# Kernel optimization log

Measured on AMD Instinct MI355X. Metric: run time of the kernel, lower is better.

## Reference

```python
import jax, jax.numpy as jnp
import numpy as np

BS, L, D, K, G, E = 512, 128, 512, 30, 8, 2048
H = E // 2  # MLP hidden = embed_dim // 2


def setup_inputs():
    key = jax.random.key(0)
    ks = jax.random.split(key, 8)
    features = jax.random.normal(ks[0], (BS, L, D), jnp.float32)
    atten = jax.random.uniform(ks[1], (BS, L, L), jnp.float32)
    rng = np.random.default_rng(0)
    lens = rng.integers(34, L - 1, size=BS)          # caption lengths (>= 34 so lengths-2 > K)
    toks = rng.integers(1, 1000, size=(BS, L))
    pos = np.arange(L)[None, :]
    text = np.where(pos < lens[:, None], toks, 0)    # zero padding
    text[np.arange(BS), lens - 1] = 49407            # eos = max token id -> argmax finds it
    text = jnp.asarray(text, jnp.int32)
    pid = jnp.asarray(np.repeat(np.arange(BS // G), G), jnp.int32)  # 64 groups of size G=8
    dlp_w = jax.random.normal(ks[2], (G, D), jnp.float32)           # weights['weight_8']
    dlp_b = jnp.zeros((G,), jnp.float32)                            # biases['bias_8']
    dlp_lw = jax.random.normal(ks[3], (K * G, E), jnp.float32) * 0.05  # linears['linear_8']
    dlp_lb = jnp.zeros((E,), jnp.float32)
    mlp_w1 = jax.random.normal(ks[4], (D, H), jnp.float32) * 0.04
    mlp_b1 = jnp.zeros((H,), jnp.float32)
    bn_g = jnp.ones((H,), jnp.float32)
    bn_b = jnp.zeros((H,), jnp.float32)
    mlp_w2 = jax.random.normal(ks[5], (H, E), jnp.float32) * 0.03
    mlp_b2 = jnp.zeros((E,), jnp.float32)
    return dict(features=features, atten=atten, text=text, pid=pid,
                dlp_w=dlp_w, dlp_b=dlp_b, dlp_lw=dlp_lw, dlp_lb=dlp_lb,
                mlp_w1=mlp_w1, mlp_b1=mlp_b1, bn_g=bn_g, bn_b=bn_b,
                mlp_w2=mlp_w2, mlp_b2=mlp_b2)


def _l2norm(x, eps=1e-8):
    return x / (jnp.sqrt(jnp.sum(x * x, axis=-1, keepdims=True)) + eps)


def _groups_from_pid(pid_np):
    # replicates the pid_dist==0 grouping + dedup-by-member-set, preserving first-seen order
    groups, order = {}, []
    for i, p in enumerate(pid_np.tolist()):
        if p not in groups:
            groups[p] = []
            order.append(p)
        groups[p].append(i)
    return [groups[p] for p in order]


def reference(features, atten, text, pid, dlp_w, dlp_b, dlp_lw, dlp_lb,
              mlp_w1, mlp_b1, bn_g, bn_b, mlp_w2, mlp_b2):
    bs = features.shape[0]
    b = jnp.arange(bs)
    mask = (text != 0).astype(features.dtype)                  # [bs, L]
    lengths = mask.sum(1) - 2.0                                # [bs]
    eos = jnp.argmax(text, axis=-1)                            # [bs]
    att = atten.at[b, :, eos].set(-1.0).at[:, :, 0].set(-1.0)
    row = att[b, eos, :] * mask                                # [bs, L]
    idx = jax.lax.top_k(row, K)[1]                             # [bs, K] topk token indices
    feats = jnp.take_along_axis(features, idx[:, :, None], axis=1)  # [bs, K, D]

    # pid-based dynamic grouping (host-side; pid is an index input, static)
    glists = _groups_from_pid(np.asarray(pid))
    assert {len(g) for g in glists} == {G}, 'expert params provided for group size G only'
    gi = np.asarray(glists)                                    # [ng, G]
    xg = feats[gi].reshape(gi.shape[0], G * K, D)              # concat group members: [ng, G*K, D]
    # F.linear(x, W[G,D], b).T  ->  [ng, G, G*K]
    h = jnp.einsum('ntd,gd->ngt', xg, dlp_w) + dlp_b[None, :, None]
    yg = h @ dlp_lw + dlp_lb                                   # linear_G: [ng, G, E]
    # scatter-combine each member's row back to its batch position
    new_base = jnp.zeros((bs, E), feats.dtype).at[gi.reshape(-1)].set(yg.reshape(-1, E))
    new_base = _l2norm(new_base)

    # MLP (Linear -> BatchNorm1d(train stats) -> ReLU -> Linear) on l2-normed gathered feats
    x = _l2norm(feats).reshape(bs * K, D) @ mlp_w1 + mlp_b1
    mu, var = x.mean(0), x.var(0)
    x = jax.nn.relu((x - mu) / jnp.sqrt(var + 1e-5) * bn_g + bn_b)
    x = (x @ mlp_w2 + mlp_b2).reshape(bs, K, E)

    # maxk_pool1d_var with pool k=1: per-channel max over first min(length, K) rows
    lens = jnp.minimum(lengths, K).astype(jnp.int32)
    valid = jnp.arange(K)[None, :] < lens[:, None]             # [bs, K]
    pooled = jnp.max(jnp.where(valid[:, :, None], x, -jnp.inf), axis=1)  # [bs, E]
    return (pooled + new_base).astype(jnp.float32)
```

## Files before the change

kernel.cpp:

```cpp
#include <hip/hip_runtime.h>
#include <hip/hip_bf16.h>

#define BS 512
#define LL 128
#define DD 512
#define KK 30
#define GG 8
#define EE 2048
#define HH 1024
#define NROWS (BS*KK)
#define NG (BS/GG)

typedef __attribute__((ext_vector_type(8))) short bf16x8;
typedef __attribute__((ext_vector_type(4))) float f32x4;
typedef __attribute__((address_space(1))) const unsigned int gu32;
typedef __attribute__((address_space(3))) unsigned int lu32;

__device__ __forceinline__ unsigned short f2bf(float f){
  unsigned int x = __float_as_uint(f);
  x = (x + 0x7FFFu + ((x >> 16) & 1u)) >> 16;
  return (unsigned short)x;
}
__device__ __forceinline__ float bf2f(unsigned short u){
  return __uint_as_float(((unsigned int)u) << 16);
}
__device__ __forceinline__ unsigned fkey(float f){
  unsigned b = __float_as_uint(f);
  return (b & 0x80000000u) ? ~b : (b | 0x80000000u);
}
__device__ __forceinline__ float fdec(unsigned k){
  unsigned b = (k & 0x80000000u) ? (k & 0x7FFFFFFFu) : ~k;
  return __uint_as_float(b);
}

__global__ __launch_bounds__(64) void k_prep(const float* __restrict__ atten,
                                             const int* __restrict__ text,
                                             int* __restrict__ idx,
                                             int* __restrict__ lensk){
  const int b = blockIdx.x;
  const int lane = threadIdx.x;
  const int t0 = text[b*LL + lane];
  const int t1 = text[b*LL + 64 + lane];

  int v, vi;
  if(t1 > t0){ v = t1; vi = lane + 64; } else { v = t0; vi = lane; }
#pragma unroll
  for(int off = 32; off; off >>= 1){
    const int ov = __shfl_xor(v, off), oi = __shfl_xor(vi, off);
    if(ov > v || (ov == v && oi < vi)){ v = ov; vi = oi; }
  }
  const int eos = vi;

  const unsigned long long mb0 = __ballot(t0 != 0), mb1 = __ballot(t1 != 0);
  if(lane == 0) lensk[b] = min(__popcll(mb0) + __popcll(mb1) - 2, KK);

  const float a0 = atten[(size_t)b*LL*LL + (size_t)eos*LL + lane];
  const float a1 = atten[(size_t)b*LL*LL + (size_t)eos*LL + 64 + lane];
  float r0 = (t0 == 0) ? 0.f : ((lane == 0 || lane == eos) ? -1.f : a0);
  float r1 = (t1 == 0) ? 0.f : ((lane + 64 == eos) ? -1.f : a1);

  for(int k = 0; k < KK; k++){
    float mv; int mi;
    if(r1 > r0){ mv = r1; mi = lane + 64; } else { mv = r0; mi = lane; }
#pragma unroll
    for(int off = 32; off; off >>= 1){
      const float ov = __shfl_xor(mv, off); const int oi = __shfl_xor(mi, off);
      if(ov > mv || (ov == mv && oi < mi)){ mv = ov; mi = oi; }
    }
    if(lane == 0) idx[b*KK + k] = mi;
    if(mi == lane)      r0 = -3.f;
    if(mi == lane + 64) r1 = -3.f;
  }
}

__global__ __launch_bounds__(128) void k_gather(const float* __restrict__ features,
                                                const float* __restrict__ dlp_w,
                                                const float* __restrict__ dlp_b,
                                                const int* __restrict__ idx,
                                                unsigned short* __restrict__ nfeats,
                                                float* __restrict__ hval){
  const int r = blockIdx.x;
  const int b = r / KK;
  const int t = threadIdx.x;
  const int l = idx[r];

  const float4 v = ((const float4*)features)[((size_t)b*LL + l)*(DD/4) + t];
  float ss = v.x*v.x + v.y*v.y + v.z*v.z + v.w*v.w;
  float hg[GG];
#pragma unroll
  for(int g = 0; g < GG; g++){
    const float4 w = ((const float4*)dlp_w)[g*(DD/4) + t];
    hg[g] = v.x*w.x + v.y*w.y + v.z*w.z + v.w*w.w;
  }
#pragma unroll
  for(int off = 32; off > 0; off >>= 1){
    ss += __shfl_down(ss, off);
#pragma unroll
    for(int g = 0; g < GG; g++) hg[g] += __shfl_down(hg[g], off);
  }
  __shared__ float red[2][9];
  __shared__ float s_rn;
  const int wave = t >> 6, lane = t & 63;
  if(lane == 0){
    red[wave][0] = ss;
#pragma unroll
    for(int g = 0; g < GG; g++) red[wave][1+g] = hg[g];
  }
  __syncthreads();
  if(t == 0) s_rn = 1.0f / (sqrtf(red[0][0] + red[1][0]) + 1e-8f);
  if(t < GG) hval[(size_t)r*GG + t] = red[0][1+t] + red[1][1+t] + dlp_b[t];
  __syncthreads();
  const float rn = s_rn;
  ushort4 u;
  u.x = f2bf(v.x*rn); u.y = f2bf(v.y*rn); u.z = f2bf(v.z*rn); u.w = f2bf(v.w*rn);
  ((ushort4*)nfeats)[(size_t)r*(DD/4) + t] = u;
}

__global__ __launch_bounds__(256) void k_dlp(const float* __restrict__ hval,
                                             const float* __restrict__ dlp_lw,
                                             const float* __restrict__ dlp_lb,
                                             unsigned short* __restrict__ nbbf){
  const int et = blockIdx.x;
  const int n  = blockIdx.y;
  const int tid = threadIdx.x;
  __shared__ float hs[GG][GG*KK];
  for(int i = tid; i < GG*GG*KK; i += 256){
    const int g = i / (GG*KK), tt = i % (GG*KK);
    const int m = tt / KK, kq = tt % KK;
    hs[g][tt] = hval[(size_t)(((n*GG + m)*KK) + kq)*GG + g];
  }
  __syncthreads();
  const int h = tid >> 7, c = tid & 127;
  const int e = et*128 + c;
  float acc[4] = {0.f, 0.f, 0.f, 0.f};
#pragma unroll 4
  for(int k = 0; k < GG*KK; k++){
    const float w = dlp_lw[(size_t)k*EE + e];
#pragma unroll
    for(int rr = 0; rr < 4; rr++) acc[rr] += hs[h*4 + rr][k] * w;
  }
  const float lb = dlp_lb[e];
#pragma unroll
  for(int rr = 0; rr < 4; rr++)
    nbbf[(size_t)(n*GG + h*4 + rr)*EE + e] = f2bf(acc[rr] + lb);
}

__global__ __launch_bounds__(256) void k_l2nb(unsigned short* __restrict__ nbbf){
  const int b = blockIdx.x, t = threadIdx.x;
  uint4* p = (uint4*)(nbbf + (size_t)b*EE);
  uint4 u = p[t];
  unsigned short* us = (unsigned short*)&u;
  float f[8]; float ss = 0.f;
#pragma unroll
  for(int j = 0; j < 8; j++){ f[j] = bf2f(us[j]); ss += f[j]*f[j]; }
#pragma unroll
  for(int off = 32; off > 0; off >>= 1) ss += __shfl_down(ss, off);
  __shared__ float red[4];
  __shared__ float s_rn;
  if((t & 63) == 0) red[t >> 6] = ss;
  __syncthreads();
  if(t == 0) s_rn = 1.0f / (sqrtf(red[0] + red[1] + red[2] + red[3]) + 1e-8f);
  __syncthreads();
  const float rn = s_rn;
#pragma unroll
  for(int j = 0; j < 8; j++) us[j] = f2bf(f[j]*rn);
  p[t] = u;
}

__global__ __launch_bounds__(256) void k_wcvt(const float* __restrict__ src,
                                              unsigned short* __restrict__ dst,
                                              int Kd, int Nd){
  __shared__ float tile[32][33];
  const int n0 = blockIdx.x*32, k0 = blockIdx.y*32;
  const int r = threadIdx.x >> 3, c4 = (threadIdx.x & 7)*4;
  const float4 v = *(const float4*)(src + (size_t)(k0 + r)*Nd + n0 + c4);
  tile[r][c4+0] = v.x; tile[r][c4+1] = v.y; tile[r][c4+2] = v.z; tile[r][c4+3] = v.w;
  __syncthreads();
  ushort4 u;
  u.x = f2bf(tile[c4+0][r]); u.y = f2bf(tile[c4+1][r]);
  u.z = f2bf(tile[c4+2][r]); u.w = f2bf(tile[c4+3][r]);
  *(ushort4*)(dst + (size_t)(n0 + r)*Kd + k0 + c4) = u;
}

template<int KD, int ND, bool POOL, bool STATS, int NBX>
__global__ __launch_bounds__(512, 2) void k_mgemm(const unsigned short* __restrict__ A,
                                                  const unsigned short* __restrict__ Bt,
                                                  const float* __restrict__ bias,
                                                  unsigned short* __restrict__ obf,
                                                  const int* __restrict__ lensk,
                                                  unsigned* __restrict__ pkey,
                                                  float* __restrict__ psum,
                                                  float* __restrict__ psq){
  __shared__ short S[2][2][256*64];
  const int tid  = threadIdx.x;
  const int wave = tid >> 6, lane = tid & 63;
  const int wr = wave >> 2, wc = wave & 3;
  const int lrow = lane & 15, kg = lane >> 4;

  const int nwg = gridDim.x, cpx = nwg >> 3;
  const int bid = (blockIdx.x & 7)*cpx + (blockIdx.x >> 3);
  const int bx = bid % NBX, by = bid / NBX;
  const int m0 = by*256, n0 = bx*256;

  const unsigned short* Ab = A  + (size_t)m0*KD;
  const unsigned short* Bb = Bt + (size_t)n0*KD;

#define STG_A(tt, p, c) { \
  const int i_ = tid + (c)*512; const int r_ = i_ >> 3; \
  const int g_ = (i_ & 7) ^ (r_ & 7); \
  __builtin_amdgcn_global_load_lds((gu32*)(Ab + (size_t)r_*KD + (tt)*64 + g_*8), \
                                   (lu32*)(&S[p][0][i_*8]), 16, 0, 0); }
#define STG_B(tt, p, c) { \
  const int i_ = tid + (c)*512; const int r_ = i_ >> 3; \
  const int g_ = (i_ & 7) ^ (r_ & 7); \
  __builtin_amdgcn_global_load_lds((gu32*)(Bb + (size_t)r_*KD + (tt)*64 + g_*8), \
                                   (lu32*)(&S[p][1][i_*8]), 16, 0, 0); }

#define DSR_B(gx)  _Pragma("unroll") for(int n = 0; n < 4; n++) \
    bg[n] = *(const bf16x8*)(Bbuf + (brow + n*16)*64 + (gx));
#define DSR_AL(gx) _Pragma("unroll") for(int m = 0; m < 4; m++) \
    af[m] = *(const bf16x8*)(Abuf + (arow + m*16)*64 + (gx));
#define DSR_AH(gx) _Pragma("unroll") for(int m = 0; m < 4; m++) \
    af[m] = *(const bf16x8*)(Abuf + (arow + 64 + m*16)*64 + (gx));
#define FENCE asm volatile("" ::: "memory")
#define BARR  do{ FENCE; __builtin_amdgcn_s_barrier(); FENCE; }while(0)
#define LGK0  do{ asm volatile("s_waitcnt lgkmcnt(0)" ::: "memory"); \
                  __builtin_amdgcn_sched_barrier(0); }while(0)
#define VMW(n) asm volatile("s_waitcnt vmcnt(" #n ")" ::: "memory")
#define MFMA_L do{ __builtin_amdgcn_s_setprio(1); \
  _Pragma("unroll") for(int m = 0; m < 4; m++) \
  _Pragma("unroll") for(int n = 0; n < 4; n++) \
    acc[m][n] = __builtin_amdgcn_mfma_f32_16x16x32_bf16(af[m], bg[n], acc[m][n], 0, 0, 0); \
  __builtin_amdgcn_s_setprio(0); }while(0)
#define MFMA_H do{ __builtin_amdgcn_s_setprio(1); \
  _Pragma("unroll") for(int m = 0; m < 4; m++) \
  _Pragma("unroll") for(int n = 0; n < 4; n++) \
    acc[4+m][n] = __builtin_amdgcn_mfma_f32_16x16x32_bf16(af[m], bg[n], acc[4+m][n], 0, 0, 0); \
  __builtin_amdgcn_s_setprio(0); }while(0)

  f32x4 acc[8][4] = {};
  const int NT = KD/64;

  const int arow = wr*128 + lrow;
  const int brow = wc*64  + lrow;
  const int gx0 = (kg       ^ (lrow & 7))*8;
  const int gx1 = ((4 + kg) ^ (lrow & 7))*8;

  STG_A(0, 0, 0) STG_A(0, 0, 2)
  STG_B(0, 0, 0) STG_B(0, 0, 1) STG_B(0, 0, 2) STG_B(0, 0, 3)
  STG_A(0, 0, 1) STG_A(0, 0, 3)
  VMW(2); BARR;

#pragma unroll 1
  for(int t = 0; t < NT-1; t++){
    const int p = t & 1, q = p ^ 1;
    const short* Abuf = &S[p][0][0];
    const short* Bbuf = &S[p][1][0];
    bf16x8 bg[4], af[4];
    DSR_B(gx0); DSR_AL(gx0);
    STG_A(t+1, q, 0) STG_A(t+1, q, 2)
    VMW(2);
    BARR; LGK0;
    MFMA_L;
    BARR;
    DSR_AH(gx0);
    STG_B(t+1, q, 0) STG_B(t+1, q, 1)
    BARR; LGK0;
    MFMA_H;
    BARR;
    DSR_B(gx1); DSR_AL(gx1);
    STG_B(t+1, q, 2) STG_B(t+1, q, 3)
    BARR; LGK0;
    MFMA_L;
    BARR;
    DSR_AH(gx1);
    STG_A(t+1, q, 1) STG_A(t+1, q, 3)
    VMW(2);
    BARR; LGK0;
    MFMA_H;
    BARR;
  }
  {
    const int p = (NT-1) & 1;
    const short* Abuf = &S[p][0][0];
    const short* Bbuf = &S[p][1][0];
    bf16x8 bg[4], af[4];
    DSR_B(gx0); DSR_AL(gx0);
    VMW(0);
    BARR; LGK0;
    MFMA_L;
    BARR;
    DSR_AH(gx0);
    BARR; LGK0;
    MFMA_H;
    BARR;
    DSR_B(gx1); DSR_AL(gx1);
    BARR; LGK0;
    MFMA_L;
    BARR;
    DSR_AH(gx1);
    LGK0;
    MFMA_H;
  }
#undef STG_A
#undef STG_B
#undef DSR_B
#undef DSR_AL
#undef DSR_AH
#undef MFMA_L
#undef MFMA_H

  if constexpr (!POOL){
    const int colb = n0 + wc*64 + lrow;
#pragma unroll
    for(int n = 0; n < 4; n++){
      const float bb = bias[colb + n*16];
      if constexpr (STATS){
        float sv = 0.f, qv = 0.f;
#pragma unroll
        for(int m = 0; m < 8; m++)
#pragma unroll
          for(int r = 0; r < 4; r++){
            const float v = acc[m][n][r] + bb; sv += v; qv += v*v;
          }
        sv += __shfl_xor(sv, 16); sv += __shfl_xor(sv, 32);
        qv += __shfl_xor(qv, 16); qv += __shfl_xor(qv, 32);
        if(lane < 16){
          psum[(size_t)(by*2 + wr)*ND + colb + n*16] = sv;
          psq [(size_t)(by*2 + wr)*ND + colb + n*16] = qv;
        }
      }
#pragma unroll
      for(int m = 0; m < 8; m++){
        const int row = m0 + wr*128 + m*16 + kg*4;
#pragma unroll
        for(int r = 0; r < 4; r++)
          obf[(size_t)(row + r)*ND + colb + n*16] = f2bf(acc[m][n][r] + bb);
      }
    }
  } else {
    __syncthreads();
    unsigned* pool = (unsigned*)&S[0][0][0];
    const int b0 = m0 / KK;
    const int b1 = (m0 + 255) / KK;
    const int nseg = b1 - b0 + 1;
    for(int i = tid; i < nseg*256; i += 512) pool[i] = 0x007FFFFFu;
    __syncthreads();
    const int lcol = wc*64 + lrow;
    {
      int cur_b = -1;
      float mx[4];
#pragma unroll
      for(int m = 0; m < 8; m++){
#pragma unroll
        for(int r = 0; r < 4; r++){
          const int row = m0 + wr*128 + m*16 + kg*4 + r;
          const int bt = row / KK;
          const int rr = row - bt*KK;
          if(bt != cur_b){
            if(cur_b >= 0){
#pragma unroll
              for(int n = 0; n < 4; n++)
                atomicMax(&pool[(cur_b - b0)*256 + lcol + n*16], fkey(mx[n]));
            }
            cur_b = bt;
#pragma unroll
            for(int n = 0; n < 4; n++) mx[n] = -INFINITY;
          }
          if(rr < lensk[bt]){
#pragma unroll
            for(int n = 0; n < 4; n++) mx[n] = fmaxf(mx[n], acc[m][n][r]);
          }
        }
      }
#pragma unroll
      for(int n = 0; n < 4; n++)
        atomicMax(&pool[(cur_b - b0)*256 + lcol + n*16], fkey(mx[n]));
    }
    __syncthreads();
    for(int e = tid; e < nseg*256; e += 512){
      const int seg = e >> 8, col = e & 255;
      atomicMax(&pkey[(size_t)(b0 + seg)*ND + n0 + col], pool[e]);
    }
  }
}

__global__ __launch_bounds__(256) void k_bnfin(const float* __restrict__ psum,
                                               const float* __restrict__ psq,
                                               const float* __restrict__ bn_g,
                                               const float* __restrict__ bn_b,
                                               float* __restrict__ sc,
                                               float* __restrict__ sh){
  const int c = blockIdx.x*256 + threadIdx.x;
  float s = 0.f, q = 0.f;
  for(int i = 0; i < 120; i++){ s += psum[(size_t)i*HH + c]; q += psq[(size_t)i*HH + c]; }
  const float mu  = s * (1.0f/NROWS);
  const float var = q * (1.0f/NROWS) - mu*mu;
  const float sv  = bn_g[c] / sqrtf(var + 1e-5f);
  sc[c] = sv;
  sh[c] = bn_b[c] - mu*sv;
}

__global__ __launch_bounds__(256) void k_bnrelu(unsigned short* __restrict__ x1,
                                                const float* __restrict__ sc,
                                                const float* __restrict__ sh,
                                                unsigned* __restrict__ pkey){
  const size_t i = (size_t)blockIdx.x*256 + threadIdx.x;
  const int c0 = (int)((i*8) & (HH-1));
  uint4 u = ((uint4*)x1)[i];
  unsigned short* us = (unsigned short*)&u;
  const float4 s0 = *(const float4*)(sc + c0), s1 = *(const float4*)(sc + c0 + 4);
  const float4 h0 = *(const float4*)(sh + c0), h1 = *(const float4*)(sh + c0 + 4);
  const float scv[8] = {s0.x,s0.y,s0.z,s0.w,s1.x,s1.y,s1.z,s1.w};
  const float shv[8] = {h0.x,h0.y,h0.z,h0.w,h1.x,h1.y,h1.z,h1.w};
#pragma unroll
  for(int j = 0; j < 8; j++)
    us[j] = f2bf(fmaxf(bf2f(us[j])*scv[j] + shv[j], 0.f));
  ((uint4*)x1)[i] = u;
  if(blockIdx.x < 1024)
    ((uint4*)pkey)[blockIdx.x*256 + threadIdx.x] =
        make_uint4(0x007FFFFFu, 0x007FFFFFu, 0x007FFFFFu, 0x007FFFFFu);
}

__global__ __launch_bounds__(256) void k_final(const unsigned* __restrict__ pkey,
                                               const float* __restrict__ b2,
                                               const unsigned short* __restrict__ nbbf,
                                               float* __restrict__ out){
  const size_t i = (size_t)blockIdx.x*256 + threadIdx.x;
  const int c0 = (int)((i*4) & (EE-1));
  const uint4 k = ((const uint4*)pkey)[i];
  const ushort4 nb4 = ((const ushort4*)nbbf)[i];
  const float4 b = *(const float4*)(b2 + c0);
  float4 o;
  o.x = fdec(k.x) + b.x + bf2f(nb4.x);
  o.y = fdec(k.y) + b.y + bf2f(nb4.y);
  o.z = fdec(k.z) + b.z + bf2f(nb4.z);
  o.w = fdec(k.w) + b.w + bf2f(nb4.w);
  ((float4*)out)[i] = o;
}

extern "C" void kernel_launch(void* const* d_in, const int* in_sizes, int n_in,
                              void* d_out, int out_size, void* d_ws, size_t ws_size,
                              hipStream_t stream){
  const float* features = (const float*)d_in[0];
  const float* atten    = (const float*)d_in[1];
  const int*   text     = (const int*)  d_in[2];
  const float* dlp_w    = (const float*)d_in[4];
  const float* dlp_b    = (const float*)d_in[5];
  const float* dlp_lw   = (const float*)d_in[6];
  const float* dlp_lb   = (const float*)d_in[7];
  const float* w1       = (const float*)d_in[8];
  const float* b1       = (const float*)d_in[9];
  const float* bn_g     = (const float*)d_in[10];
  const float* bn_b     = (const float*)d_in[11];
  const float* w2       = (const float*)d_in[12];
  const float* b2       = (const float*)d_in[13];
  float* out = (float*)d_out;

  char* ws = (char*)d_ws;
  float*          psum   = (float*)(ws + 0);
  float*          psq    = (float*)(ws + 983040);
  unsigned short* w1t    = (unsigned short*)(ws + 1966080);
  float*          hval   = (float*)(ws + 3014656);
  int*            idx    = (int*)(ws + 3506176);
  unsigned*       pkey   = (unsigned*)(ws + 0);
  int*            lensk  = (int*)(ws + 4194304);
  float*          sc     = (float*)(ws + 4196352);
  float*          sh     = (float*)(ws + 4200448);
  unsigned short* nfeats = (unsigned short*)(ws + 4204544);
  unsigned short* w2t    = (unsigned short*)(ws + 4204544);
  unsigned short* x1     = (unsigned short*)(ws + 19933184);
  unsigned short* nbbf   = (unsigned short*)(ws + 51390464);

  k_wcvt<<<dim3(HH/32, DD/32), 256, 0, stream>>>(w1, w1t, DD, HH);
  k_prep<<<BS, 64, 0, stream>>>(atten, text, idx, lensk);
  k_gather<<<NROWS, 128, 0, stream>>>(features, dlp_w, dlp_b, idx, nfeats, hval);
  k_dlp<<<dim3(16, NG), 256, 0, stream>>>(hval, dlp_lw, dlp_lb, nbbf);
  k_l2nb<<<BS, 256, 0, stream>>>(nbbf);
  k_mgemm<DD, HH, false, true, HH/256><<<(HH/256)*(NROWS/256), 512, 0, stream>>>(
      nfeats, w1t, b1, x1, nullptr, nullptr, psum, psq);
  k_wcvt<<<dim3(EE/32, HH/32), 256, 0, stream>>>(w2, w2t, HH, EE);
  k_bnfin<<<4, 256, 0, stream>>>(psum, psq, bn_g, bn_b, sc, sh);
  k_bnrelu<<<(NROWS*HH/8)/256, 256, 0, stream>>>(x1, sc, sh, pkey);
  k_mgemm<HH, EE, true, false, EE/256><<<(EE/256)*(NROWS/256), 512, 0, stream>>>(
      x1, w2t, nullptr, nullptr, lensk, pkey, nullptr, nullptr);
  k_final<<<(BS*EE/4)/256, 256, 0, stream>>>(pkey, b2, nbbf, out);
}
```

Baseline: 213.0 us.

## Fuse prep/gather/weight-convert kernels and retile first GEMM to 128x128

Merges token selection, feature gather and W1 conversion into one launch, keeping the top-K indices in shared memory instead of a global round-trip. It also merges the BN finalize with the W2 conversion. The first GEMM gets its own 128x128, 256-thread kernel with a simpler double-buffered loop, giving more workgroups for the small K=512 GEMM. The second GEMM is split out as a dedicated non-templated kernel. This cuts launch count and improves occupancy for GEMM1, at the cost of more partial-stat rows (240) to reduce and a less aggressive pipeline in GEMM1.

```diff
diff --git a/kernel.cpp b/kernel.cpp
--- a/kernel.cpp
+++ b/kernel.cpp
@@ -33,87 +33,105 @@
   return __uint_as_float(b);
 }
 
-__global__ __launch_bounds__(64) void k_prep(const float* __restrict__ atten,
-                                             const int* __restrict__ text,
-                                             int* __restrict__ idx,
-                                             int* __restrict__ lensk){
+#define FENCE asm volatile("" ::: "memory")
+#define BARR  do{ FENCE; __builtin_amdgcn_s_barrier(); FENCE; }while(0)
+#define LGK0  do{ asm volatile("s_waitcnt lgkmcnt(0)" ::: "memory"); \
+                  __builtin_amdgcn_sched_barrier(0); }while(0)
+#define VMW(n) asm volatile("s_waitcnt vmcnt(" #n ")" ::: "memory")
+
+__global__ __launch_bounds__(256) void k_pg(const float* __restrict__ atten,
+                                            const int* __restrict__ text,
+                                            const float* __restrict__ features,
+                                            const float* __restrict__ dlp_w,
+                                            const float* __restrict__ dlp_b,
+                                            const float* __restrict__ w1,
+                                            unsigned short* __restrict__ w1t,
+                                            unsigned short* __restrict__ nfeats,
+                                            float* __restrict__ hval,
+                                            int* __restrict__ lensk){
+  __shared__ int sidx[KK];
+  __shared__ float tile[32][33];
+
+  if(blockIdx.x >= BS){
+    const int blk = blockIdx.x - BS;
+    const int n0 = (blk & 31)*32, k0 = (blk >> 5)*32;
+    const int r = threadIdx.x >> 3, c4 = (threadIdx.x & 7)*4;
+    const float4 v = *(const float4*)(w1 + (size_t)(k0 + r)*HH + n0 + c4);
+    tile[r][c4+0] = v.x; tile[r][c4+1] = v.y; tile[r][c4+2] = v.z; tile[r][c4+3] = v.w;
+    __syncthreads();
+    ushort4 u;
+    u.x = f2bf(tile[c4+0][r]); u.y = f2bf(tile[c4+1][r]);
+    u.z = f2bf(tile[c4+2][r]); u.w = f2bf(tile[c4+3][r]);
+    *(ushort4*)(w1t + (size_t)(n0 + r)*DD + k0 + c4) = u;
+    return;
+  }
+
   const int b = blockIdx.x;
-  const int lane = threadIdx.x;
-  const int t0 = text[b*LL + lane];
-  const int t1 = text[b*LL + 64 + lane];
-
-  int v, vi;
-  if(t1 > t0){ v = t1; vi = lane + 64; } else { v = t0; vi = lane; }
-#pragma unroll
-  for(int off = 32; off; off >>= 1){
-    const int ov = __shfl_xor(v, off), oi = __shfl_xor(vi, off);
-    if(ov > v || (ov == v && oi < vi)){ v = ov; vi = oi; }
-  }
-  const int eos = vi;
-
-  const unsigned long long mb0 = __ballot(t0 != 0), mb1 = __ballot(t1 != 0);
-  if(lane == 0) lensk[b] = min(__popcll(mb0) + __popcll(mb1) - 2, KK);
-
-  const float a0 = atten[(size_t)b*LL*LL + (size_t)eos*LL + lane];
-  const float a1 = atten[(size_t)b*LL*LL + (size_t)eos*LL + 64 + lane];
-  float r0 = (t0 == 0) ? 0.f : ((lane == 0 || lane == eos) ? -1.f : a0);
-  float r1 = (t1 == 0) ? 0.f : ((lane + 64 == eos) ? -1.f : a1);
-
-  for(int k = 0; k < KK; k++){
-    float mv; int mi;
-    if(r1 > r0){ mv = r1; mi = lane + 64; } else { mv = r0; mi = lane; }
+  const int tid = threadIdx.x;
+  const int wv = tid >> 6, lane = tid & 63;
+
+  if(wv == 0){
+    const int t0 = text[b*LL + lane];
+    const int t1 = text[b*LL + 64 + lane];
+    int v, vi;
+    if(t1 > t0){ v = t1; vi = lane + 64; } else { v = t0; vi = lane; }
 #pragma unroll
     for(int off = 32; off; off >>= 1){
-      const float ov = __shfl_xor(mv, off); const int oi = __shfl_xor(mi, off);
-      if(ov > mv || (ov == mv && oi < mi)){ mv = ov; mi = oi; }
+      const int ov = __shfl_xor(v, off), oi = __shfl_xor(vi, off);
+      if(ov > v || (ov == v && oi < vi)){ v = ov; vi = oi; }
     }
-    if(lane == 0) idx[b*KK + k] = mi;
-    if(mi == lane)      r0 = -3.f;
-    if(mi == lane + 64) r1 = -3.f;
-  }
-}
-
-__global__ __launch_bounds__(128) void k_gather(const float* __restrict__ features,
-                                                const float* __restrict__ dlp_w,
-                                                const float* __restrict__ dlp_b,
-                                                const int* __restrict__ idx,
-                                                unsigned short* __restrict__ nfeats,
-                                                float* __restrict__ hval){
-  const int r = blockIdx.x;
-  const int b = r / KK;
-  const int t = threadIdx.x;
-  const int l = idx[r];
-
-  const float4 v = ((const float4*)features)[((size_t)b*LL + l)*(DD/4) + t];
-  float ss = v.x*v.x + v.y*v.y + v.z*v.z + v.w*v.w;
-  float hg[GG];
-#pragma unroll
-  for(int g = 0; g < GG; g++){
-    const float4 w = ((const float4*)dlp_w)[g*(DD/4) + t];
-    hg[g] = v.x*w.x + v.y*w.y + v.z*w.z + v.w*w.w;
-  }
-#pragma unroll
-  for(int off = 32; off > 0; off >>= 1){
-    ss += __shfl_down(ss, off);
-#pragma unroll
-    for(int g = 0; g < GG; g++) hg[g] += __shfl_down(hg[g], off);
-  }
-  __shared__ float red[2][9];
-  __shared__ float s_rn;
-  const int wave = t >> 6, lane = t & 63;
-  if(lane == 0){
-    red[wave][0] = ss;
-#pragma unroll
-    for(int g = 0; g < GG; g++) red[wave][1+g] = hg[g];
-  }
-  __syncthreads();
-  if(t == 0) s_rn = 1.0f / (sqrtf(red[0][0] + red[1][0]) + 1e-8f);
-  if(t < GG) hval[(size_t)r*GG + t] = red[0][1+t] + red[1][1+t] + dlp_b[t];
-  __syncthreads();
-  const float rn = s_rn;
-  ushort4 u;
-  u.x = f2bf(v.x*rn); u.y = f2bf(v.y*rn); u.z = f2bf(v.z*rn); u.w = f2bf(v.w*rn);
-  ((ushort4*)nfeats)[(size_t)r*(DD/4) + t] = u;
+    const int eos = vi;
+    const unsigned long long mb0 = __ballot(t0 != 0), mb1 = __ballot(t1 != 0);
+    if(lane == 0) lensk[b] = min(__popcll(mb0) + __popcll(mb1) - 2, KK);
+
+    const float a0 = atten[(size_t)b*LL*LL + (size_t)eos*LL + lane];
+    const float a1 = atten[(size_t)b*LL*LL + (size_t)eos*LL + 64 + lane];
+    float r0 = (t0 == 0) ? 0.f : ((lane == 0 || lane == eos) ? -1.f : a0);
+    float r1 = (t1 == 0) ? 0.f : ((lane + 64 == eos) ? -1.f : a1);
+    for(int k = 0; k < KK; k++){
+      float mv; int mi;
+      if(r1 > r0){ mv = r1; mi = lane + 64; } else { mv = r0; mi = lane; }
+#pragma unroll
+      for(int off = 32; off; off >>= 1){
+        const float ov = __shfl_xor(mv, off); const int oi = __shfl_xor(mi, off);
+        if(ov > mv || (ov == mv && oi < mi)){ mv = ov; mi = oi; }
+      }
+      if(lane == 0) sidx[k] = mi;
+      if(mi == lane)      r0 = -3.f;
+      if(mi == lane + 64) r1 = -3.f;
+    }
+  }
+  __syncthreads();
+
+  for(int it = 0; it < 8; it++){
+    const int r = it*4 + wv;
+    if(r >= KK) break;
+    const int l = sidx[r];
+    const float4* fp = (const float4*)features + ((size_t)b*LL + l)*(DD/4);
+    const float4 v0 = fp[lane], v1 = fp[64 + lane];
+    float ss = v0.x*v0.x + v0.y*v0.y + v0.z*v0.z + v0.w*v0.w
+             + v1.x*v1.x + v1.y*v1.y + v1.z*v1.z + v1.w*v1.w;
+#pragma unroll
+    for(int off = 32; off; off >>= 1) ss += __shfl_xor(ss, off);
+    float hout = 0.f;
+#pragma unroll
+    for(int g = 0; g < GG; g++){
+      const float4 w0 = ((const float4*)dlp_w)[g*(DD/4) + lane];
+      const float4 w1v = ((const float4*)dlp_w)[g*(DD/4) + 64 + lane];
+      float hg = v0.x*w0.x + v0.y*w0.y + v0.z*w0.z + v0.w*w0.w
+               + v1.x*w1v.x + v1.y*w1v.y + v1.z*w1v.z + v1.w*w1v.w;
+#pragma unroll
+      for(int off = 32; off; off >>= 1) hg += __shfl_xor(hg, off);
+      if(lane == g) hout = hg;
+    }
+    if(lane < GG) hval[(size_t)(b*KK + r)*GG + lane] = hout + dlp_b[lane];
+    const float rn = 1.0f / (sqrtf(ss) + 1e-8f);
+    ushort4 u0, u1;
+    u0.x = f2bf(v0.x*rn); u0.y = f2bf(v0.y*rn); u0.z = f2bf(v0.z*rn); u0.w = f2bf(v0.w*rn);
+    u1.x = f2bf(v1.x*rn); u1.y = f2bf(v1.y*rn); u1.z = f2bf(v1.z*rn); u1.w = f2bf(v1.w*rn);
+    ushort4* np = (ushort4*)nfeats + (size_t)(b*KK + r)*(DD/4);
+    np[lane] = u0; np[64 + lane] = u1;
+  }
 }
 
 __global__ __launch_bounds__(256) void k_dlp(const float* __restrict__ hval,
@@ -167,238 +185,147 @@
   p[t] = u;
 }
 
-__global__ __launch_bounds__(256) void k_wcvt(const float* __restrict__ src,
-                                              unsigned short* __restrict__ dst,
-                                              int Kd, int Nd){
+__global__ __launch_bounds__(256, 2) void k_g1(const unsigned short* __restrict__ A,
+                                               const unsigned short* __restrict__ Bt,
+                                               const float* __restrict__ bias,
+                                               unsigned short* __restrict__ obf,
+                                               float* __restrict__ psum,
+                                               float* __restrict__ psq){
+  const int KD = DD, ND = HH, NBX = HH/128;
+  __shared__ short S[2][2][128*64];
+  const int tid  = threadIdx.x;
+  const int wave = tid >> 6, lane = tid & 63;
+  const int wr = wave >> 1, wc = wave & 1;
+  const int lrow = lane & 15, kg = lane >> 4;
+
+  const int nwg = gridDim.x, cpx = nwg >> 3;
+  const int bid = (blockIdx.x & 7)*cpx + (blockIdx.x >> 3);
+  const int bx = bid % NBX, by = bid / NBX;
+  const int m0 = by*128, n0 = bx*128;
+
+  const unsigned short* Ab = A  + (size_t)m0*KD;
+  const unsigned short* Bb = Bt + (size_t)n0*KD;
+
+#define G1STG(tt, p) { \
+  _Pragma("unroll") \
+  for(int c = 0; c < 4; c++){ \
+    const int i_ = tid + c*256; const int r_ = i_ >> 3; \
+    const int g_ = (i_ & 7) ^ (r_ & 7); \
+    __builtin_amdgcn_global_load_lds((gu32*)(Ab + (size_t)r_*KD + (tt)*64 + g_*8), \
+                                     (lu32*)(&S[p][0][i_*8]), 16, 0, 0); \
+  } \
+  _Pragma("unroll") \
+  for(int c = 0; c < 4; c++){ \
+    const int i_ = tid + c*256; const int r_ = i_ >> 3; \
+    const int g_ = (i_ & 7) ^ (r_ & 7); \
+    __builtin_amdgcn_global_load_lds((gu32*)(Bb + (size_t)r_*KD + (tt)*64 + g_*8), \
+                                     (lu32*)(&S[p][1][i_*8]), 16, 0, 0); \
+  } \
+}
+
+  f32x4 acc[4][4] = {};
+  const int NT = KD/64;
+  G1STG(0, 0)
+  G1STG(1, 1)
+
+  const int arow = wr*64 + lrow;
+  const int brow = wc*64 + lrow;
+  const int gx0 = (kg       ^ (lrow & 7))*8;
+  const int gx1 = ((4 + kg) ^ (lrow & 7))*8;
+
+#pragma unroll 1
+  for(int t = 0; t < NT; t++){
+    const int p = t & 1;
+    if(t < NT-1) VMW(8);
+    else         VMW(0);
+    BARR;
+    const short* Abuf = &S[p][0][0];
+    const short* Bbuf = &S[p][1][0];
+    bf16x8 af[4], bg[4];
+#pragma unroll
+    for(int n = 0; n < 4; n++) bg[n] = *(const bf16x8*)(Bbuf + (brow + n*16)*64 + gx0);
+#pragma unroll
+    for(int m = 0; m < 4; m++) af[m] = *(const bf16x8*)(Abuf + (arow + m*16)*64 + gx0);
+    __builtin_amdgcn_s_setprio(1);
+#pragma unroll
+    for(int m = 0; m < 4; m++)
+#pragma unroll
+      for(int n = 0; n < 4; n++)
+        acc[m][n] = __builtin_amdgcn_mfma_f32_16x16x32_bf16(af[m], bg[n], acc[m][n], 0, 0, 0);
+    __builtin_amdgcn_s_setprio(0);
+#pragma unroll
+    for(int n = 0; n < 4; n++) bg[n] = *(const bf16x8*)(Bbuf + (brow + n*16)*64 + gx1);
+#pragma unroll
+    for(int m = 0; m < 4; m++) af[m] = *(const bf16x8*)(Abuf + (arow + m*16)*64 + gx1);
+    __builtin_amdgcn_s_setprio(1);
+#pragma unroll
+    for(int m = 0; m < 4; m++)
+#pragma unroll
+      for(int n = 0; n < 4; n++)
+        acc[m][n] = __builtin_amdgcn_mfma_f32_16x16x32_bf16(af[m], bg[n], acc[m][n], 0, 0, 0);
+    __builtin_amdgcn_s_setprio(0);
+    BARR;
+    if(t + 2 < NT){ G1STG(t+2, p) }
+  }
+#undef G1STG
+
+  const int colb = n0 + wc*64 + lrow;
+#pragma unroll
+  for(int n = 0; n < 4; n++){
+    const float bb = bias[colb + n*16];
+    float sv = 0.f, qv = 0.f;
+#pragma unroll
+    for(int m = 0; m < 4; m++)
+#pragma unroll
+      for(int r = 0; r < 4; r++){
+        const float v = acc[m][n][r] + bb; sv += v; qv += v*v;
+      }
+    sv += __shfl_xor(sv, 16); sv += __shfl_xor(sv, 32);
+    qv += __shfl_xor(qv, 16); qv += __shfl_xor(qv, 32);
+    if(lane < 16){
+      psum[(size_t)(by*2 + wr)*ND + colb + n*16] = sv;
+      psq [(size_t)(by*2 + wr)*ND + colb + n*16] = qv;
+    }
+#pragma unroll
+    for(int m = 0; m < 4; m++){
+      const int row = m0 + wr*64 + m*16 + kg*4;
+#pragma unroll
+      for(int r = 0; r < 4; r++)
+        obf[(size_t)(row + r)*ND + colb + n*16] = f2bf(acc[m][n][r] + bb);
+    }
+  }
+}
+
+__global__ __launch_bounds__(256) void k_bnw(const float* __restrict__ psum,
+                                             const float* __restrict__ psq,
+                                             const float* __restrict__ bn_g,
+                                             const float* __restrict__ bn_b,
+                                             float* __restrict__ sc,
+                                             float* __restrict__ sh,
+                                             const float* __restrict__ w2,
+                                             unsigned short* __restrict__ w2t){
+  if(blockIdx.x < 4){
+    const int c = blockIdx.x*256 + threadIdx.x;
+    float s = 0.f, q = 0.f;
+    for(int i = 0; i < 240; i++){ s += psum[(size_t)i*HH + c]; q += psq[(size_t)i*HH + c]; }
+    const float mu  = s * (1.0f/NROWS);
+    const float var = q * (1.0f/NROWS) - mu*mu;
+    const float sv  = bn_g[c] / sqrtf(var + 1e-5f);
+    sc[c] = sv;
+    sh[c] = bn_b[c] - mu*sv;
+    return;
+  }
   __shared__ float tile[32][33];
-  const int n0 = blockIdx.x*32, k0 = blockIdx.y*32;
+  const int blk = blockIdx.x - 4;
+  const int n0 = (blk & 63)*32, k0 = (blk >> 6)*32;
   const int r = threadIdx.x >> 3, c4 = (threadIdx.x & 7)*4;
-  const float4 v = *(const float4*)(src + (size_t)(k0 + r)*Nd + n0 + c4);
+  const float4 v = *(const float4*)(w2 + (size_t)(k0 + r)*EE + n0 + c4);
   tile[r][c4+0] = v.x; tile[r][c4+1] = v.y; tile[r][c4+2] = v.z; tile[r][c4+3] = v.w;
   __syncthreads();
   ushort4 u;
   u.x = f2bf(tile[c4+0][r]); u.y = f2bf(tile[c4+1][r]);
   u.z = f2bf(tile[c4+2][r]); u.w = f2bf(tile[c4+3][r]);
-  *(ushort4*)(dst + (size_t)(n0 + r)*Kd + k0 + c4) = u;
-}
-
-template<int KD, int ND, bool POOL, bool STATS, int NBX>
-__global__ __launch_bounds__(512, 2) void k_mgemm(const unsigned short* __restrict__ A,
-                                                  const unsigned short* __restrict__ Bt,
-                                                  const float* __restrict__ bias,
-                                                  unsigned short* __restrict__ obf,
-                                                  const int* __restrict__ lensk,
-                                                  unsigned* __restrict__ pkey,
-                                                  float* __restrict__ psum,
-                                                  float* __restrict__ psq){
-  __shared__ short S[2][2][256*64];
-  const int tid  = threadIdx.x;
-  const int wave = tid >> 6, lane = tid & 63;
-  const int wr = wave >> 2, wc = wave & 3;
-  const int lrow = lane & 15, kg = lane >> 4;
-
-  const int nwg = gridDim.x, cpx = nwg >> 3;
-  const int bid = (blockIdx.x & 7)*cpx + (blockIdx.x >> 3);
-  const int bx = bid % NBX, by = bid / NBX;
-  const int m0 = by*256, n0 = bx*256;
-
-  const unsigned short* Ab = A  + (size_t)m0*KD;
-  const unsigned short* Bb = Bt + (size_t)n0*KD;
-
-#define STG_A(tt, p, c) { \
-  const int i_ = tid + (c)*512; const int r_ = i_ >> 3; \
-  const int g_ = (i_ & 7) ^ (r_ & 7); \
-  __builtin_amdgcn_global_load_lds((gu32*)(Ab + (size_t)r_*KD + (tt)*64 + g_*8), \
-                                   (lu32*)(&S[p][0][i_*8]), 16, 0, 0); }
-#define STG_B(tt, p, c) { \
-  const int i_ = tid + (c)*512; const int r_ = i_ >> 3; \
-  const int g_ = (i_ & 7) ^ (r_ & 7); \
-  __builtin_amdgcn_global_load_lds((gu32*)(Bb + (size_t)r_*KD + (tt)*64 + g_*8), \
-                                   (lu32*)(&S[p][1][i_*8]), 16, 0, 0); }
-
-#define DSR_B(gx)  _Pragma("unroll") for(int n = 0; n < 4; n++) \
-    bg[n] = *(const bf16x8*)(Bbuf + (brow + n*16)*64 + (gx));
-#define DSR_AL(gx) _Pragma("unroll") for(int m = 0; m < 4; m++) \
-    af[m] = *(const bf16x8*)(Abuf + (arow + m*16)*64 + (gx));
-#define DSR_AH(gx) _Pragma("unroll") for(int m = 0; m < 4; m++) \
-    af[m] = *(const bf16x8*)(Abuf + (arow + 64 + m*16)*64 + (gx));
-#define FENCE asm volatile("" ::: "memory")
-#define BARR  do{ FENCE; __builtin_amdgcn_s_barrier(); FENCE; }while(0)
-#define LGK0  do{ asm volatile("s_waitcnt lgkmcnt(0)" ::: "memory"); \
-                  __builtin_amdgcn_sched_barrier(0); }while(0)
-#define VMW(n) asm volatile("s_waitcnt vmcnt(" #n ")" ::: "memory")
-#define MFMA_L do{ __builtin_amdgcn_s_setprio(1); \
-  _Pragma("unroll") for(int m = 0; m < 4; m++) \
-  _Pragma("unroll") for(int n = 0; n < 4; n++) \
-    acc[m][n] = __builtin_amdgcn_mfma_f32_16x16x32_bf16(af[m], bg[n], acc[m][n], 0, 0, 0); \
-  __builtin_amdgcn_s_setprio(0); }while(0)
-#define MFMA_H do{ __builtin_amdgcn_s_setprio(1); \
-  _Pragma("unroll") for(int m = 0; m < 4; m++) \
-  _Pragma("unroll") for(int n = 0; n < 4; n++) \
-    acc[4+m][n] = __builtin_amdgcn_mfma_f32_16x16x32_bf16(af[m], bg[n], acc[4+m][n], 0, 0, 0); \
-  __builtin_amdgcn_s_setprio(0); }while(0)
-
-  f32x4 acc[8][4] = {};
-  const int NT = KD/64;
-
-  const int arow = wr*128 + lrow;
-  const int brow = wc*64  + lrow;
-  const int gx0 = (kg       ^ (lrow & 7))*8;
-  const int gx1 = ((4 + kg) ^ (lrow & 7))*8;
-
-  STG_A(0, 0, 0) STG_A(0, 0, 2)
-  STG_B(0, 0, 0) STG_B(0, 0, 1) STG_B(0, 0, 2) STG_B(0, 0, 3)
-  STG_A(0, 0, 1) STG_A(0, 0, 3)
-  VMW(2); BARR;
-
-#pragma unroll 1
-  for(int t = 0; t < NT-1; t++){
-    const int p = t & 1, q = p ^ 1;
-    const short* Abuf = &S[p][0][0];
-    const short* Bbuf = &S[p][1][0];
-    bf16x8 bg[4], af[4];
-    DSR_B(gx0); DSR_AL(gx0);
-    STG_A(t+1, q, 0) STG_A(t+1, q, 2)
-    VMW(2);
-    BARR; LGK0;
-    MFMA_L;
-    BARR;
-    DSR_AH(gx0);
-    STG_B(t+1, q, 0) STG_B(t+1, q, 1)
-    BARR; LGK0;
-    MFMA_H;
-    BARR;
-    DSR_B(gx1); DSR_AL(gx1);
-    STG_B(t+1, q, 2) STG_B(t+1, q, 3)
-    BARR; LGK0;
-    MFMA_L;
-    BARR;
-    DSR_AH(gx1);
-    STG_A(t+1, q, 1) STG_A(t+1, q, 3)
-    VMW(2);
-    BARR; LGK0;
-    MFMA_H;
-    BARR;
-  }
-  {
-    const int p = (NT-1) & 1;
-    const short* Abuf = &S[p][0][0];
-    const short* Bbuf = &S[p][1][0];
-    bf16x8 bg[4], af[4];
-    DSR_B(gx0); DSR_AL(gx0);
-    VMW(0);
-    BARR; LGK0;
-    MFMA_L;
-    BARR;
-    DSR_AH(gx0);
-    BARR; LGK0;
-    MFMA_H;
-    BARR;
-    DSR_B(gx1); DSR_AL(gx1);
-    BARR; LGK0;
-    MFMA_L;
-    BARR;
-    DSR_AH(gx1);
-    LGK0;
-    MFMA_H;
-  }
-#undef STG_A
-#undef STG_B
-#undef DSR_B
-#undef DSR_AL
-#undef DSR_AH
-#undef MFMA_L
-#undef MFMA_H
-
-  if constexpr (!POOL){
-    const int colb = n0 + wc*64 + lrow;
-#pragma unroll
-    for(int n = 0; n < 4; n++){
-      const float bb = bias[colb + n*16];
-      if constexpr (STATS){
-        float sv = 0.f, qv = 0.f;
-#pragma unroll
-        for(int m = 0; m < 8; m++)
-#pragma unroll
-          for(int r = 0; r < 4; r++){
-            const float v = acc[m][n][r] + bb; sv += v; qv += v*v;
-          }
-        sv += __shfl_xor(sv, 16); sv += __shfl_xor(sv, 32);
-        qv += __shfl_xor(qv, 16); qv += __shfl_xor(qv, 32);
-        if(lane < 16){
-          psum[(size_t)(by*2 + wr)*ND + colb + n*16] = sv;
-          psq [(size_t)(by*2 + wr)*ND + colb + n*16] = qv;
-        }
-      }
-#pragma unroll
-      for(int m = 0; m < 8; m++){
-        const int row = m0 + wr*128 + m*16 + kg*4;
-#pragma unroll
-        for(int r = 0; r < 4; r++)
-          obf[(size_t)(row + r)*ND + colb + n*16] = f2bf(acc[m][n][r] + bb);
-      }
-    }
-  } else {
-    __syncthreads();
-    unsigned* pool = (unsigned*)&S[0][0][0];
-    const int b0 = m0 / KK;
-    const int b1 = (m0 + 255) / KK;
-    const int nseg = b1 - b0 + 1;
-    for(int i = tid; i < nseg*256; i += 512) pool[i] = 0x007FFFFFu;
-    __syncthreads();
-    const int lcol = wc*64 + lrow;
-    {
-      int cur_b = -1;
-      float mx[4];
-#pragma unroll
-      for(int m = 0; m < 8; m++){
-#pragma unroll
-        for(int r = 0; r < 4; r++){
-          const int row = m0 + wr*128 + m*16 + kg*4 + r;
-          const int bt = row / KK;
-          const int rr = row - bt*KK;
-          if(bt != cur_b){
-            if(cur_b >= 0){
-#pragma unroll
-              for(int n = 0; n < 4; n++)
-                atomicMax(&pool[(cur_b - b0)*256 + lcol + n*16], fkey(mx[n]));
-            }
-            cur_b = bt;
-#pragma unroll
-            for(int n = 0; n < 4; n++) mx[n] = -INFINITY;
-          }
-          if(rr < lensk[bt]){
-#pragma unroll
-            for(int n = 0; n < 4; n++) mx[n] = fmaxf(mx[n], acc[m][n][r]);
-          }
-        }
-      }
-#pragma unroll
-      for(int n = 0; n < 4; n++)
-        atomicMax(&pool[(cur_b - b0)*256 + lcol + n*16], fkey(mx[n]));
-    }
-    __syncthreads();
-    for(int e = tid; e < nseg*256; e += 512){
-      const int seg = e >> 8, col = e & 255;
-      atomicMax(&pkey[(size_t)(b0 + seg)*ND + n0 + col], pool[e]);
-    }
-  }
-}
-
-__global__ __launch_bounds__(256) void k_bnfin(const float* __restrict__ psum,
-                                               const float* __restrict__ psq,
-                                               const float* __restrict__ bn_g,
-                                               const float* __restrict__ bn_b,
-                                               float* __restrict__ sc,
-                                               float* __restrict__ sh){
-  const int c = blockIdx.x*256 + threadIdx.x;
-  float s = 0.f, q = 0.f;
-  for(int i = 0; i < 120; i++){ s += psum[(size_t)i*HH + c]; q += psq[(size_t)i*HH + c]; }
-  const float mu  = s * (1.0f/NROWS);
-  const float var = q * (1.0f/NROWS) - mu*mu;
-  const float sv  = bn_g[c] / sqrtf(var + 1e-5f);
-  sc[c] = sv;
-  sh[c] = bn_b[c] - mu*sv;
+  *(ushort4*)(w2t + (size_t)(n0 + r)*HH + k0 + c4) = u;
 }
 
 __global__ __launch_bounds__(256) void k_bnrelu(unsigned short* __restrict__ x1,
@@ -420,6 +347,169 @@
   if(blockIdx.x < 1024)
     ((uint4*)pkey)[blockIdx.x*256 + threadIdx.x] =
         make_uint4(0x007FFFFFu, 0x007FFFFFu, 0x007FFFFFu, 0x007FFFFFu);
+}
+
+__global__ __launch_bounds__(512, 2) void k_g2(const unsigned short* __restrict__ A,
+                                               const unsigned short* __restrict__ Bt,
+                                               const int* __restrict__ lensk,
+                                               unsigned* __restrict__ pkey){
+  const int KD = HH, ND = EE, NBX = EE/256;
+  __shared__ short S[2][2][256*64];
+  const int tid  = threadIdx.x;
+  const int wave = tid >> 6, lane = tid & 63;
+  const int wr = wave >> 2, wc = wave & 3;
+  const int lrow = lane & 15, kg = lane >> 4;
+
+  const int nwg = gridDim.x, cpx = nwg >> 3;
+  const int bid = (blockIdx.x & 7)*cpx + (blockIdx.x >> 3);
+  const int bx = bid % NBX, by = bid / NBX;
+  const int m0 = by*256, n0 = bx*256;
+
+  const unsigned short* Ab = A  + (size_t)m0*KD;
+  const unsigned short* Bb = Bt + (size_t)n0*KD;
+
+#define STG_A(tt, p, c) { \
+  const int i_ = tid + (c)*512; const int r_ = i_ >> 3; \
+  const int g_ = (i_ & 7) ^ (r_ & 7); \
+  __builtin_amdgcn_global_load_lds((gu32*)(Ab + (size_t)r_*KD + (tt)*64 + g_*8), \
+                                   (lu32*)(&S[p][0][i_*8]), 16, 0, 0); }
+#define STG_B(tt, p, c) { \
+  const int i_ = tid + (c)*512; const int r_ = i_ >> 3; \
+  const int g_ = (i_ & 7) ^ (r_ & 7); \
+  __builtin_amdgcn_global_load_lds((gu32*)(Bb + (size_t)r_*KD + (tt)*64 + g_*8), \
+                                   (lu32*)(&S[p][1][i_*8]), 16, 0, 0); }
+#define DSR_B(gx)  _Pragma("unroll") for(int n = 0; n < 4; n++) \
+    bg[n] = *(const bf16x8*)(Bbuf + (brow + n*16)*64 + (gx));
+#define DSR_AL(gx) _Pragma("unroll") for(int m = 0; m < 4; m++) \
+    af[m] = *(const bf16x8*)(Abuf + (arow + m*16)*64 + (gx));
+#define DSR_AH(gx) _Pragma("unroll") for(int m = 0; m < 4; m++) \
+    af[m] = *(const bf16x8*)(Abuf + (arow + 64 + m*16)*64 + (gx));
+#define MFMA_L do{ __builtin_amdgcn_s_setprio(1); \
+  _Pragma("unroll") for(int m = 0; m < 4; m++) \
+  _Pragma("unroll") for(int n = 0; n < 4; n++) \
+    acc[m][n] = __builtin_amdgcn_mfma_f32_16x16x32_bf16(af[m], bg[n], acc[m][n], 0, 0, 0); \
+  __builtin_amdgcn_s_setprio(0); }while(0)
+#define MFMA_H do{ __builtin_amdgcn_s_setprio(1); \
+  _Pragma("unroll") for(int m = 0; m < 4; m++) \
+  _Pragma("unroll") for(int n = 0; n < 4; n++) \
+    acc[4+m][n] = __builtin_amdgcn_mfma_f32_16x16x32_bf16(af[m], bg[n], acc[4+m][n], 0, 0, 0); \
+  __builtin_amdgcn_s_setprio(0); }while(0)
+
+  f32x4 acc[8][4] = {};
+  const int NT = KD/64;
+
+  const int arow = wr*128 + lrow;
+  const int brow = wc*64  + lrow;
+  const int gx0 = (kg       ^ (lrow & 7))*8;
+  const int gx1 = ((4 + kg) ^ (lrow & 7))*8;
+
+  STG_A(0, 0, 0) STG_A(0, 0, 2)
+  STG_B(0, 0, 0) STG_B(0, 0, 1) STG_B(0, 0, 2) STG_B(0, 0, 3)
+  STG_A(0, 0, 1) STG_A(0, 0, 3)
+  VMW(2); BARR;
+
+#pragma unroll 1
+  for(int t = 0; t < NT-1; t++){
+    const int p = t & 1, q = p ^ 1;
+    const short* Abuf = &S[p][0][0];
+    const short* Bbuf = &S[p][1][0];
+    bf16x8 bg[4], af[4];
+    DSR_B(gx0); DSR_AL(gx0);
+    STG_A(t+1, q, 0) STG_A(t+1, q, 2)
+    VMW(2);
+    BARR; LGK0;
+    MFMA_L;
+    BARR;
+    DSR_AH(gx0);
+    STG_B(t+1, q, 0) STG_B(t+1, q, 1)
+    BARR; LGK0;
+    MFMA_H;
+    BARR;
+    DSR_B(gx1); DSR_AL(gx1);
+    STG_B(t+1, q, 2) STG_B(t+1, q, 3)
+    BARR; LGK0;
+    MFMA_L;
+    BARR;
+    DSR_AH(gx1);
+    STG_A(t+1, q, 1) STG_A(t+1, q, 3)
+    VMW(2);
+    BARR; LGK0;
+    MFMA_H;
+    BARR;
+  }
+  {
+    const int p = (NT-1) & 1;
+    const short* Abuf = &S[p][0][0];
+    const short* Bbuf = &S[p][1][0];
+    bf16x8 bg[4], af[4];
+    DSR_B(gx0); DSR_AL(gx0);
+    VMW(0);
+    BARR; LGK0;
+    MFMA_L;
+    BARR;
+    DSR_AH(gx0);
+    BARR; LGK0;
+    MFMA_H;
+    BARR;
+    DSR_B(gx1); DSR_AL(gx1);
+    BARR; LGK0;
+    MFMA_L;
+    BARR;
+    DSR_AH(gx1);
+    LGK0;
+    MFMA_H;
+  }
+#undef STG_A
+#undef STG_B
+#undef DSR_B
+#undef DSR_AL
+#undef DSR_AH
+#undef MFMA_L
+#undef MFMA_H
+
+  __syncthreads();
+  unsigned* pool = (unsigned*)&S[0][0][0];
+  const int b0 = m0 / KK;
+  const int b1 = (m0 + 255) / KK;
+  const int nseg = b1 - b0 + 1;
+  for(int i = tid; i < nseg*256; i += 512) pool[i] = 0x007FFFFFu;
+  __syncthreads();
+  const int lcol = wc*64 + lrow;
+  {
+    int cur_b = -1;
+    float mx[4];
+#pragma unroll
+    for(int m = 0; m < 8; m++){
+#pragma unroll
+      for(int r = 0; r < 4; r++){
+        const int row = m0 + wr*128 + m*16 + kg*4 + r;
+        const int bt = row / KK;
+        const int rr = row - bt*KK;
+        if(bt != cur_b){
+          if(cur_b >= 0){
+#pragma unroll
+            for(int n = 0; n < 4; n++)
+              atomicMax(&pool[(cur_b - b0)*256 + lcol + n*16], fkey(mx[n]));
+          }
+          cur_b = bt;
+#pragma unroll
+          for(int n = 0; n < 4; n++) mx[n] = -INFINITY;
+        }
+        if(rr < lensk[bt]){
+#pragma unroll
+          for(int n = 0; n < 4; n++) mx[n] = fmaxf(mx[n], acc[m][n][r]);
+        }
+      }
+    }
+#pragma unroll
+    for(int n = 0; n < 4; n++)
+      atomicMax(&pool[(cur_b - b0)*256 + lcol + n*16], fkey(mx[n]));
+  }
+  __syncthreads();
+  for(int e = tid; e < nseg*256; e += 512){
+    const int seg = e >> 8, col = e & 255;
+    atomicMax(&pkey[(size_t)(b0 + seg)*ND + n0 + col], pool[e]);
+  }
 }
 
 __global__ __launch_bounds__(256) void k_final(const unsigned* __restrict__ pkey,
@@ -462,7 +552,6 @@
   float*          psq    = (float*)(ws + 983040);
   unsigned short* w1t    = (unsigned short*)(ws + 1966080);
   float*          hval   = (float*)(ws + 3014656);
-  int*            idx    = (int*)(ws + 3506176);
   unsigned*       pkey   = (unsigned*)(ws + 0);
   int*            lensk  = (int*)(ws + 4194304);
   float*          sc     = (float*)(ws + 4196352);
@@ -472,17 +561,13 @@
   unsigned short* x1     = (unsigned short*)(ws + 19933184);
   unsigned short* nbbf   = (unsigned short*)(ws + 51390464);
 
-  k_wcvt<<<dim3(HH/32, DD/32), 256, 0, stream>>>(w1, w1t, DD, HH);
-  k_prep<<<BS, 64, 0, stream>>>(atten, text, idx, lensk);
-  k_gather<<<NROWS, 128, 0, stream>>>(features, dlp_w, dlp_b, idx, nfeats, hval);
+  k_pg<<<BS + 512, 256, 0, stream>>>(atten, text, features, dlp_w, dlp_b,
+                                     w1, w1t, nfeats, hval, lensk);
   k_dlp<<<dim3(16, NG), 256, 0, stream>>>(hval, dlp_lw, dlp_lb, nbbf);
   k_l2nb<<<BS, 256, 0, stream>>>(nbbf);
-  k_mgemm<DD, HH, false, true, HH/256><<<(HH/256)*(NROWS/256), 512, 0, stream>>>(
-      nfeats, w1t, b1, x1, nullptr, nullptr, psum, psq);
-  k_wcvt<<<dim3(EE/32, HH/32), 256, 0, stream>>>(w2, w2t, HH, EE);
-  k_bnfin<<<4, 256, 0, stream>>>(psum, psq, bn_g, bn_b, sc, sh);
+  k_g1<<<(HH/128)*(NROWS/128), 256, 0, stream>>>(nfeats, w1t, b1, x1, psum, psq);
+  k_bnw<<<4 + 2048, 256, 0, stream>>>(psum, psq, bn_g, bn_b, sc, sh, w2, w2t);
   k_bnrelu<<<(NROWS*HH/8)/256, 256, 0, stream>>>(x1, sc, sh, pkey);
-  k_mgemm<HH, EE, true, false, EE/256><<<(EE/256)*(NROWS/256), 512, 0, stream>>>(
-      x1, w2t, nullptr, nullptr, lensk, pkey, nullptr, nullptr);
+  k_g2<<<(EE/256)*(NROWS/256), 512, 0, stream>>>(x1, w2t, lensk, pkey);
   k_final<<<(BS*EE/4)/256, 256, 0, stream>>>(pkey, b2, nbbf, out);
 }
```

Result: faster. 183.0 us (-14.1%).
